# Kernel optimization log

Measured on AMD Instinct MI355X. Metric: run time of the kernel, lower is better.

## Reference

```python
import jax, jax.numpy as jnp
import numpy as np

EMBED_DIM = 768
NUM_HEADS = 12
HEAD_DIM = EMBED_DIM // NUM_HEADS
B, S = 2, 2048


def setup_inputs() -> dict:
    key = jax.random.key(0)
    ks = jax.random.split(key, 6)
    glorot = jnp.sqrt(6.0 / (EMBED_DIM + EMBED_DIM)).astype(jnp.float32)
    x = jax.random.normal(ks[0], (B, S, EMBED_DIM), dtype=jnp.float32)
    mask = jnp.zeros((1, 1, S, S), dtype=jnp.float32)  # additive mask, 0 = no masking
    Wq = jax.random.uniform(ks[1], (EMBED_DIM, EMBED_DIM), jnp.float32, -glorot, glorot)
    Wk = jax.random.uniform(ks[2], (EMBED_DIM, EMBED_DIM), jnp.float32, -glorot, glorot)
    Wv = jax.random.uniform(ks[3], (EMBED_DIM, EMBED_DIM), jnp.float32, -glorot, glorot)
    Wo = jax.random.uniform(ks[4], (EMBED_DIM, EMBED_DIM), jnp.float32, -glorot, glorot)
    bo = jnp.zeros((EMBED_DIM,), dtype=jnp.float32)
    return {"x": x, "mask": mask, "Wq": Wq, "Wk": Wk, "Wv": Wv, "Wo": Wo, "bo": bo}


def reference(x, mask, Wq, Wk, Wv, Wo, bo):
    b, s, _ = x.shape
    # Q/K/V projections (no bias), split into heads: [b, h, s, d]
    def split_heads(t):
        return t.reshape(b, s, NUM_HEADS, HEAD_DIM).transpose(0, 2, 1, 3)
    q = split_heads(x @ Wq)
    k = split_heads(x @ Wk)
    v = split_heads(x @ Wv)
    scale = 1.0 / jnp.sqrt(jnp.float32(HEAD_DIM))
    logits = jnp.einsum('bhqd,bhkd->bhqk', q, k) * scale  # [b, h, s, s]
    logits = logits + mask * (-1e9)
    weights = jax.nn.softmax(logits, axis=-1)
    attn = jnp.einsum('bhqk,bhkd->bhqd', weights, v)
    concat = attn.transpose(0, 2, 1, 3).reshape(b, s, EMBED_DIM)
    return concat @ Wo + bo
```

## Files before the change

### kernel.cpp

```cpp
#include <hip/hip_runtime.h>


typedef __bf16 bf16_t;
typedef bf16_t bf16x8 __attribute__((ext_vector_type(8)));
typedef bf16_t bf16x4 __attribute__((ext_vector_type(4)));
typedef float f32x4 __attribute__((ext_vector_type(4)));
typedef _Float16 f16x4 __attribute__((ext_vector_type(4)));
typedef _Float16 f16x8 __attribute__((ext_vector_type(8)));
typedef __fp16 hf2 __attribute__((ext_vector_type(2)));

#define SC2 0.1803368801111137f
#define DEFER_THR 44.0f

__device__ __forceinline__ float bf2f(unsigned short u) {
  union { unsigned int i; float f; } x;
  x.i = ((unsigned int)u) << 16;
  return x.f;
}

__device__ __forceinline__ float fexp2(float x) {
  return __builtin_amdgcn_exp2f(x);
}

__device__ __forceinline__ void glds16(const bf16_t* g, bf16_t* l) {
  __builtin_amdgcn_global_load_lds(
      (const __attribute__((address_space(1))) void*)g,
      (__attribute__((address_space(3))) void*)l, 16, 0, 0);
}

__device__ __forceinline__ int detect_bf16_flag(const unsigned short* x) {
  const int lane = threadIdx.x & 63;
  const uint4* p = (const uint4*)x;
  uint4 a = p[lane * 2];
  uint4 b = p[lane * 2 + 1];
  unsigned int w[8] = {a.x, a.y, a.z, a.w, b.x, b.y, b.z, b.w};
  unsigned int big = 0;
#pragma unroll
  for (int i = 0; i < 8; i++) {
    unsigned int e0 = (w[i] >> 7) & 0xFF, e1 = (w[i] >> 23) & 0xFF;
    big |= (e0 > 0x88u) | (e1 > 0x88u);
  }
  unsigned long long bal = __ballot(big != 0u);
  return bal == 0ULL ? 1 : 0;
}

__global__ void k_prep(const void* __restrict__ x, const void* __restrict__ mask,
                       const void* __restrict__ Wq, const void* __restrict__ Wk,
                       const void* __restrict__ Wv, const void* __restrict__ Wo,
                       bf16_t* __restrict__ xb, bf16_t* __restrict__ wqkvT,
                       bf16_t* __restrict__ woT, int* __restrict__ mflags) {
  __shared__ float ts[32][33];
  __shared__ int snz;
  const int blk = blockIdx.x;
  const int f = detect_bf16_flag((const unsigned short*)x);

  if (blk < 1536) {
    if (f) return;
    int i = blk * 256 + threadIdx.x;
    const float* xf = (const float*)x + (size_t)i * 8;
    bf16x8 v;
#pragma unroll
    for (int j = 0; j < 8; j++) v[j] = (bf16_t)xf[j];
    *(bf16x8*)(xb + (size_t)i * 8) = v;
  } else if (blk < 3840) {
    const int t = blk - 1536;
    const int z = t / 576, r = t % 576, kt = r / 24, nt = r % 24;
    const void* wsrc = (z == 0) ? Wq : (z == 1) ? Wk : (z == 2) ? Wv : Wo;
    bf16_t* dst = (z < 3) ? (wqkvT + (size_t)z * 768 * 768) : woT;
    const int c = threadIdx.x & 31, r0 = threadIdx.x >> 5;
#pragma unroll
    for (int i = 0; i < 4; i++) {
      int kr = kt * 32 + r0 + i * 8;
      float v;
      if (f) v = bf2f(((const unsigned short*)wsrc)[(size_t)kr * 768 + nt * 32 + c]);
      else   v = ((const float*)wsrc)[(size_t)kr * 768 + nt * 32 + c];
      ts[r0 + i * 8][c] = v;
    }
    __syncthreads();
#pragma unroll
    for (int i = 0; i < 4; i++) {
      int nr = nt * 32 + r0 + i * 8;
      dst[(size_t)nr * 768 + kt * 32 + c] = (bf16_t)ts[c][r0 + i * 8];
    }
  } else {
    const int t = blk - 3840;
    const int qt = t >> 4, ktm = t & 15;
    if (threadIdx.x == 0) snz = 0;
    __syncthreads();
    unsigned int nz = 0;
    if (f) {
#pragma unroll
      for (int i = 0; i < 8; i++) {
        int uidx = i * 256 + threadIdx.x;
        int row = uidx >> 4, col = uidx & 15;
        const uint4* p = (const uint4*)((const char*)mask +
            ((size_t)(qt * 128 + row) * 2048 + ktm * 128) * 2 + col * 16);
        uint4 v = *p;
        nz |= ((v.x | v.y | v.z | v.w) & 0x7fff7fffu);
      }
    } else {
#pragma unroll
      for (int i = 0; i < 16; i++) {
        int uidx = i * 256 + threadIdx.x;
        int row = uidx >> 5, col = uidx & 31;
        const uint4* p = (const uint4*)((const char*)mask +
            ((size_t)(qt * 128 + row) * 2048 + ktm * 128) * 4 + col * 16);
        uint4 v = *p;
        nz |= ((v.x | v.y | v.z | v.w) & 0x7fffffffu);
      }
    }
    if (nz) snz = 1;
    __syncthreads();
    if (threadIdx.x == 0) mflags[qt * 16 + ktm] = snz;
  }
}

__global__ __launch_bounds__(256, 3) void k_gemmQKV(
    const bf16_t* __restrict__ xb, const bf16_t* __restrict__ Bm,
    bf16_t* __restrict__ Qd, bf16_t* __restrict__ Kd, _Float16* __restrict__ Vt,
    const unsigned short* __restrict__ xdet) {
  __shared__ __align__(16) char smem[32768];
  _Float16* Tb = (_Float16*)smem;

  const int f = detect_bf16_flag(xdet);
  const bf16_t* A = f ? (const bf16_t*)xdet : xb;

  const int tid = threadIdx.x;
  const int n0 = blockIdx.x * 128, m0 = blockIdx.y * 128;
  const int r = tid >> 2, c8 = (tid & 3) << 3;
  const bf16_t* Ag = A + (size_t)(m0 + r) * 768 + c8;
  const bf16_t* Bg = Bm + (size_t)(n0 + r) * 768 + c8;
  const int wid = tid >> 6, lane = tid & 63;
  const int wm = (wid >> 1) << 6, wn = (wid & 1) << 6;
  const int lr = lane & 15, lk = (lane >> 4) << 3, g4 = (lane >> 4) << 2;

  f32x4 acc[4][4];
  const f32x4 z = {0.f, 0.f, 0.f, 0.f};
#pragma unroll
  for (int i = 0; i < 4; i++)
#pragma unroll
    for (int j = 0; j < 4; j++) acc[i][j] = z;

  {
    bf16_t* A0 = (bf16_t*)smem;
    bf16_t* B0 = (bf16_t*)(smem + 16384);
    glds16(Ag, A0 + wid * 512);
    glds16(Ag + (size_t)64 * 768, A0 + 2048 + wid * 512);
    glds16(Bg, B0 + wid * 512);
    glds16(Bg + (size_t)64 * 768, B0 + 2048 + wid * 512);
  }
  __syncthreads();

  for (int s = 0; s < 24; s++) {
    if (s < 23) {
      const int k0 = (s + 1) * 32;
      bf16_t* An = (bf16_t*)(smem + ((s + 1) & 1) * 8192);
      bf16_t* Bn = (bf16_t*)(smem + 16384 + ((s + 1) & 1) * 8192);
      glds16(Ag + k0, An + wid * 512);
      glds16(Ag + (size_t)64 * 768 + k0, An + 2048 + wid * 512);
      glds16(Bg + k0, Bn + wid * 512);
      glds16(Bg + (size_t)64 * 768 + k0, Bn + 2048 + wid * 512);
    }
    const bf16_t* As = (const bf16_t*)(smem + (s & 1) * 8192);
    const bf16_t* Bs = (const bf16_t*)(smem + 16384 + (s & 1) * 8192);
    bf16x8 af[4], bf_[4];
#pragma unroll
    for (int t = 0; t < 4; t++) af[t]  = *(const bf16x8*)&As[(wm + t * 16 + lr) * 32 + lk];
#pragma unroll
    for (int t = 0; t < 4; t++) bf_[t] = *(const bf16x8*)&Bs[(wn + t * 16 + lr) * 32 + lk];
#pragma unroll
    for (int i = 0; i < 4; i++)
#pragma unroll
      for (int j = 0; j < 4; j++)
        acc[i][j] = __builtin_amdgcn_mfma_f32_16x16x32_bf16(af[i], bf_[j], acc[i][j], 0, 0, 0);
    __syncthreads();
  }

  if (n0 < 1536) {
    bf16_t* dst = (n0 < 768) ? Qd : Kd;
    const int nb = (n0 < 768) ? n0 : n0 - 768;
    const int bb = m0 >> 11;
#pragma unroll
    for (int i = 0; i < 4; i++)
#pragma unroll
      for (int j = 0; j < 4; j++) {
        const int rc = nb + wn + j * 16 + lr;
        const int hh = rc >> 6, dd = rc & 63;
        const size_t base = (((size_t)bb * 12 + hh) * 2048) * 64 + dd;
#pragma unroll
        for (int reg = 0; reg < 4; reg++) {
          const int s = (m0 & 2047) + wm + i * 16 + g4 + reg;
          dst[base + (size_t)s * 64] = (bf16_t)acc[i][j][reg];
        }
      }
  } else {
    const int bb = m0 >> 11;
#pragma unroll
    for (int half = 0; half < 2; half++) {
      if ((wid & 1) == half) {
#pragma unroll
        for (int j = 0; j < 4; j++) {
          const int d_l = j * 16 + lr;
#pragma unroll
          for (int i = 0; i < 4; i++)
#pragma unroll
            for (int reg = 0; reg < 4; reg++)
              Tb[d_l * 136 + wm + i * 16 + g4 + reg] = (_Float16)acc[i][j][reg];
        }
      }
      __syncthreads();
      const int row = tid >> 2, cc = (tid & 3) * 32;
      const int vcol = (n0 - 1536) + half * 64 + row;
      const int hh = vcol >> 6;
      _Float16* dstv = Vt + (((size_t)bb * 12 + hh) * 64 + row) * 2048 + (m0 & 2047) + cc;
#pragma unroll
      for (int u = 0; u < 4; u++)
        *(uint4*)(dstv + u * 8) = *(const uint4*)&Tb[row * 136 + cc + u * 8];
      __syncthreads();
    }
  }
}

__global__ __launch_bounds__(320, 4) void k_flash(
    const bf16_t* __restrict__ Qd, const bf16_t* __restrict__ Kd,
    const _Float16* __restrict__ Vt, const void* __restrict__ mask,
    const int* __restrict__ mflags, const unsigned short* __restrict__ xdet,
    bf16_t* __restrict__ attn) {
  __shared__ __align__(16) char sm[32768];

  const int tid = threadIdx.x, wid = tid >> 6, lane = tid & 63;
  const int lr = lane & 15, quad = lane >> 4, lk = quad << 3, g4 = quad << 2;

  const int lin = blockIdx.x;
  const int gx = lin & 7, ww = lin >> 3;
  const int hb = gx * 3 + (ww >> 5);
  const int h = hb % 12, bb = hb / 12;
  const int qt = ww & 31;

  const size_t bh = (size_t)bb * 12 + h;
  const char* Kh = (const char*)(Kd + bh * 2048 * 64);
  const char* Vh = (const char*)(Vt + bh * 64 * 2048);

  if (wid == 4) {
    const char* kS[8]; const char* vS[8];
    int kL[8], vL[8];
#pragma unroll
    for (int u = 0; u < 8; u++) {
      const int R = (u >> 1) * 16 + lr;
      const int cG = (u & 1) * 4 + quad;
      kS[u] = Kh + R * 128 + cG * 16;
      const int s = ((u >> 2) << 5) + (((lr >> 2) & 1) << 4) +
                    (((u >> 1) & 1) << 3) + ((lr >> 3) << 2) + (lr & 3);
      kL[u] = (s >> 4) * 2048 + (cG & 3) * 256 + (s & 15) * 16 + (cG >> 2) * 1024;
      vS[u] = Vh + (size_t)lane * 4096 + u * 16;
      vL[u] = 8192 + lane * 128 + ((u * 16) ^ ((lane & 7) << 4));
    }
    uint4 kv[8], vv[8];
#pragma unroll
    for (int u = 0; u < 8; u++) kv[u] = *(const uint4*)(kS[u]);
#pragma unroll
    for (int u = 0; u < 8; u++) vv[u] = *(const uint4*)(vS[u]);
#pragma unroll
    for (int u = 0; u < 8; u++) *(uint4*)(sm + kL[u]) = kv[u];
#pragma unroll
    for (int u = 0; u < 8; u++) *(uint4*)(sm + vL[u]) = vv[u];
    __syncthreads();
    for (int s = 0; s < 32; s++) {
      if (s < 31) {
        const int t = s + 1;
        char* buf = sm + (t & 1) * 16384;
#pragma unroll
        for (int u = 0; u < 8; u++) kv[u] = *(const uint4*)(kS[u] + (size_t)t * 8192);
#pragma unroll
        for (int u = 0; u < 8; u++) vv[u] = *(const uint4*)(vS[u] + (size_t)t * 128);
#pragma unroll
        for (int u = 0; u < 8; u++) *(uint4*)(buf + kL[u]) = kv[u];
#pragma unroll
        for (int u = 0; u < 8; u++) *(uint4*)(buf + vL[u]) = vv[u];
      }
      __syncthreads();
    }
    return;
  }

  const bf16_t* Qh = Qd + bh * 2048 * 64;
  const int q0 = qt * 64 + wid * 16;
  const int mbf = detect_bf16_flag(xdet);
  const int* mfrow = mflags + (qt >> 1) * 16;
  int mbits = 0;
#pragma unroll
  for (int t = 0; t < 16; t++) mbits |= (mfrow[t] != 0) << t;

  const bf16x8 qf0 = *(const bf16x8*)&Qh[(size_t)(q0 + lr) * 64 + lk];
  const bf16x8 qf1 = *(const bf16x8*)&Qh[(size_t)(q0 + lr) * 64 + 32 + lk];

  f16x8 ones8;
#pragma unroll
  for (int j = 0; j < 8; j++) ones8[j] = (_Float16)1.f;

  const int vxo0 = (quad * 16) ^ ((lr & 7) << 4);
  const int vxo1 = (64 + quad * 16) ^ ((lr & 7) << 4);

  const f32x4 z = {0.f, 0.f, 0.f, 0.f};
  f32x4 ot[4];
#pragma unroll
  for (int dt = 0; dt < 4; dt++) ot[dt] = z;
  float mrow = -1e30f, lrow = 0.f;

  __syncthreads();

  for (int s = 0; s < 32; s++) {
    const char* Kc = sm + (s & 1) * 16384;
    const char* Vc = Kc + 8192;

    f32x4 sv[4];
#pragma unroll
    for (int ct = 0; ct < 4; ct++) sv[ct] = z;
    __builtin_amdgcn_s_setprio(1);
#pragma unroll
    for (int ct = 0; ct < 4; ct++) {
      bf16x8 kf0 = *(const bf16x8*)(Kc + ct * 2048 + lane * 16);
      bf16x8 kf1 = *(const bf16x8*)(Kc + ct * 2048 + 1024 + lane * 16);
      sv[ct] = __builtin_amdgcn_mfma_f32_16x16x32_bf16(kf0, qf0, sv[ct], 0, 0, 0);
      sv[ct] = __builtin_amdgcn_mfma_f32_16x16x32_bf16(kf1, qf1, sv[ct], 0, 0, 0);
    }
    __builtin_amdgcn_s_setprio(0);

    if ((mbits >> (s >> 1)) & 1) {
#pragma unroll
      for (int ct = 0; ct < 4; ct++)
#pragma unroll
        for (int reg = 0; reg < 4; reg++) {
          const int kk = ((ct >> 1) << 5) + (quad << 3) + ((ct & 1) << 2) + reg;
          size_t mi = (size_t)(q0 + lr) * 2048 + s * 64 + kk;
          float mv = mbf ? bf2f(((const unsigned short*)mask)[mi])
                         : ((const float*)mask)[mi];
          sv[ct][reg] -= 8e9f * mv;
        }
    }

    float t = fmaxf(
        fmaxf(fmaxf(fmaxf(sv[0][0], sv[0][1]), fmaxf(sv[0][2], sv[0][3])),
              fmaxf(fmaxf(sv[1][0], sv[1][1]), fmaxf(sv[1][2], sv[1][3]))),
        fmaxf(fmaxf(fmaxf(sv[2][0], sv[2][1]), fmaxf(sv[2][2], sv[2][3])),
              fmaxf(fmaxf(sv[3][0], sv[3][1]), fmaxf(sv[3][2], sv[3][3]))));
    t = fmaxf(t, __shfl_xor(t, 16));
    t = fmaxf(t, __shfl_xor(t, 32));
    if (__ballot(t > mrow + DEFER_THR)) {
      const float mnew = fmaxf(mrow, t);
      const float alpha = fexp2((mrow - mnew) * SC2);
#pragma unroll
      for (int dt = 0; dt < 4; dt++)
#pragma unroll
        for (int reg = 0; reg < 4; reg++) ot[dt][reg] *= alpha;
      lrow *= alpha;
      mrow = mnew;
    }
    const float mS = mrow * SC2;

    f16x8 pb8[2];
#pragma unroll
    for (int c2 = 0; c2 < 2; c2++) {
      union { hf2 h[4]; f16x8 v; } u;
#pragma unroll
      for (int hh2 = 0; hh2 < 2; hh2++) {
        const int ct = c2 * 2 + hh2;
        float p0 = fexp2(fmaf(sv[ct][0], SC2, -mS));
        float p1 = fexp2(fmaf(sv[ct][1], SC2, -mS));
        float p2 = fexp2(fmaf(sv[ct][2], SC2, -mS));
        float p3 = fexp2(fmaf(sv[ct][3], SC2, -mS));
        u.h[hh2 * 2 + 0] = __builtin_amdgcn_cvt_pkrtz(p0, p1);
        u.h[hh2 * 2 + 1] = __builtin_amdgcn_cvt_pkrtz(p2, p3);
      }
      pb8[c2] = u.v;
    }

    f32x4 asum = z;
    __builtin_amdgcn_s_setprio(1);
#pragma unroll
    for (int c2 = 0; c2 < 2; c2++) {
      const int vxo = c2 ? vxo1 : vxo0;
      asum = __builtin_amdgcn_mfma_f32_16x16x32_f16(ones8, pb8[c2], asum, 0, 0, 0);
#pragma unroll
      for (int dt = 0; dt < 4; dt++) {
        f16x8 va = *(const f16x8*)(Vc + (dt * 16 + lr) * 128 + vxo);
        ot[dt] = __builtin_amdgcn_mfma_f32_16x16x32_f16(va, pb8[c2], ot[dt], 0, 0, 0);
      }
    }
    __builtin_amdgcn_s_setprio(0);
    lrow += asum[0];
    __syncthreads();
  }

  const float inv = 1.0f / lrow;
  bf16_t* arow = attn + ((size_t)bb * 2048 + q0 + lr) * 768 + h * 64 + g4;
#pragma unroll
  for (int dt = 0; dt < 4; dt++) {
    bf16x4 v;
#pragma unroll
    for (int reg = 0; reg < 4; reg++) v[reg] = (bf16_t)(ot[dt][reg] * inv);
    *(bf16x4*)(arow + dt * 16) = v;
  }
}

__global__ __launch_bounds__(256, 3) void k_gemm2(
    const bf16_t* __restrict__ A, const bf16_t* __restrict__ Bm,
    const void* __restrict__ bo, const unsigned short* __restrict__ xdet,
    float* __restrict__ outF, unsigned short* __restrict__ outH) {
  __shared__ __align__(16) char smem[32768];

  const int tid = threadIdx.x, wid = tid >> 6, lane = tid & 63;
  const int n0 = blockIdx.x * 64, m0 = blockIdx.y * 64;
  const int wm = (wid >> 1) << 5, wn = (wid & 1) << 5;
  const int lr = lane & 15, lk = (lane >> 4) << 3, g4 = (lane >> 4) << 2;
  const bf16_t* Ag = A + (size_t)(m0 + (tid >> 2)) * 768 + ((tid & 3) << 3);
  const bf16_t* Bg = Bm + (size_t)(n0 + (tid >> 2)) * 768 + ((tid & 3) << 3);

  f32x4 acc[2][2];
  const f32x4 z = {0.f, 0.f, 0.f, 0.f};
#pragma unroll
  for (int i = 0; i < 2; i++)
#pragma unroll
    for (int j = 0; j < 2; j++) acc[i][j] = z;

  {
    bf16_t* A0 = (bf16_t*)smem;
    bf16_t* B0 = (bf16_t*)(smem + 16384);
    glds16(Ag, A0 + wid * 512);
    glds16(Ag + 32, A0 + 2048 + wid * 512);
    glds16(Bg, B0 + wid * 512);
    glds16(Bg + 32, B0 + 2048 + wid * 512);
  }
  __syncthreads();

  for (int s = 0; s < 12; s++) {
    if (s < 11) {
      const int k0 = (s + 1) * 64;
      bf16_t* An = (bf16_t*)(smem + ((s + 1) & 1) * 8192);
      bf16_t* Bn = (bf16_t*)(smem + 16384 + ((s + 1) & 1) * 8192);
      glds16(Ag + k0, An + wid * 512);
      glds16(Ag + k0 + 32, An + 2048 + wid * 512);
      glds16(Bg + k0, Bn + wid * 512);
      glds16(Bg + k0 + 32, Bn + 2048 + wid * 512);
    }
#pragma unroll
    for (int kc = 0; kc < 2; kc++) {
      const bf16_t* As = (const bf16_t*)(smem + (s & 1) * 8192) + kc * 2048;
      const bf16_t* Bs = (const bf16_t*)(smem + 16384 + (s & 1) * 8192) + kc * 2048;
      bf16x8 af[2], bf_[2];
#pragma unroll
      for (int i = 0; i < 2; i++) af[i]  = *(const bf16x8*)&As[(wm + i * 16 + lr) * 32 + lk];
#pragma unroll
      for (int j = 0; j < 2; j++) bf_[j] = *(const bf16x8*)&Bs[(wn + j * 16 + lr) * 32 + lk];
#pragma unroll
      for (int i = 0; i < 2; i++)
#pragma unroll
        for (int j = 0; j < 2; j++)
          acc[i][j] = __builtin_amdgcn_mfma_f32_16x16x32_bf16(af[i], bf_[j], acc[i][j], 0, 0, 0);
    }
    __syncthreads();
  }

  const int obf = detect_bf16_flag(xdet);
#pragma unroll
  for (int i = 0; i < 2; i++)
#pragma unroll
    for (int j = 0; j < 2; j++) {
      const int nn = n0 + wn + j * 16 + lr;
      const float bv = obf ? bf2f(((const unsigned short*)bo)[nn])
                           : ((const float*)bo)[nn];
#pragma unroll
      for (int reg = 0; reg < 4; reg++) {
        const int m = m0 + wm + i * 16 + g4 + reg;
        const float v = acc[i][j][reg] + bv;
        if (obf) outH[(size_t)m * 768 + nn] = __builtin_bit_cast(unsigned short, (bf16_t)v);
        else     outF[(size_t)m * 768 + nn] = v;
      }
    }
}

extern "C" void kernel_launch(void* const* d_in, const int* in_sizes, int n_in,
                              void* d_out, int out_size, void* d_ws, size_t ws_size,
                              hipStream_t stream) {
  (void)in_sizes; (void)n_in; (void)out_size; (void)ws_size;
  const void* x    = d_in[0];
  const void* mask = d_in[1];
  const void* Wq   = d_in[2];
  const void* Wk   = d_in[3];
  const void* Wv   = d_in[4];
  const void* Wo   = d_in[5];
  const void* bo   = d_in[6];

  char* w = (char*)d_ws;
  size_t off = 0;
  auto take = [&](size_t b) -> void* {
    void* p = w + off;
    off = (off + b + 255) & ~(size_t)255;
    return p;
  };
  int*      mflags = (int*)take(256 * 4);
  bf16_t*   wqkvT  = (bf16_t*)take((size_t)2304 * 768 * 2);
  bf16_t*   woT    = (bf16_t*)take((size_t)768 * 768 * 2);
  bf16_t*   xb     = (bf16_t*)take((size_t)4096 * 768 * 2);
  bf16_t*   Qd     = (bf16_t*)take((size_t)3145728 * 2);
  bf16_t*   Kd     = (bf16_t*)take((size_t)3145728 * 2);
  _Float16* Vt     = (_Float16*)take((size_t)3145728 * 2);
  bf16_t*   attn   = xb;

  k_prep<<<4096, 256, 0, stream>>>(x, mask, Wq, Wk, Wv, Wo, xb, wqkvT, woT, mflags);
  k_gemmQKV<<<dim3(18, 32), 256, 0, stream>>>(xb, wqkvT, Qd, Kd, Vt,
                                              (const unsigned short*)x);
  k_flash<<<768, 320, 0, stream>>>(Qd, Kd, Vt, mask, mflags,
                                   (const unsigned short*)x, attn);
  k_gemm2<<<dim3(12, 64), 256, 0, stream>>>(attn, woT, bo, (const unsigned short*)x,
                                            (float*)d_out, (unsigned short*)d_out);
}
```

Before: 178.1 us.

## Pre-swizzle K/V tiles in QKV GEMM epilogue and load via direct-to-LDS copies

The QKV GEMM epilogue now writes K and V into a tile-major layout that exactly matches the shared-memory layout the flash kernel consumes, including the swizzle. This lets the flash kernel drop its dedicated producer wave, which loaded into registers and stored to LDS, and instead have all four compute waves issue contiguous global-to-LDS 16-byte copies for the next tile. The intent is to cut the block from 320 to 256 threads, remove the register round trip and scattered address math, and let loads overlap compute through double buffering. In exchange, the GEMM epilogue now does scattered 2-byte stores for K, and the prefetch is issued by the compute waves themselves.

```diff
diff --git a/kernel.cpp b/kernel.cpp
--- a/kernel.cpp
+++ b/kernel.cpp
@@ -117,7 +117,7 @@
 
 __global__ __launch_bounds__(256, 3) void k_gemmQKV(
     const bf16_t* __restrict__ xb, const bf16_t* __restrict__ Bm,
-    bf16_t* __restrict__ Qd, bf16_t* __restrict__ Kd, _Float16* __restrict__ Vt,
+    bf16_t* __restrict__ Qd, char* __restrict__ Kd, char* __restrict__ Vt,
     const unsigned short* __restrict__ xdet) {
   __shared__ __align__(16) char smem[32768];
   _Float16* Tb = (_Float16*)smem;
@@ -132,7 +132,7 @@
   const bf16_t* Bg = Bm + (size_t)(n0 + r) * 768 + c8;
   const int wid = tid >> 6, lane = tid & 63;
   const int wm = (wid >> 1) << 6, wn = (wid & 1) << 6;
-  const int lr = lane & 15, lk = (lane >> 4) << 3, g4 = (lane >> 4) << 2;
+  const int lr = lane & 15, quad = lane >> 4, lk = quad << 3, g4 = quad << 2;
 
   f32x4 acc[4][4];
   const f32x4 z = {0.f, 0.f, 0.f, 0.f};
@@ -176,23 +176,42 @@
     __syncthreads();
   }
 
-  if (n0 < 1536) {
-    bf16_t* dst = (n0 < 768) ? Qd : Kd;
-    const int nb = (n0 < 768) ? n0 : n0 - 768;
+  if (n0 < 768) {
     const int bb = m0 >> 11;
 #pragma unroll
     for (int i = 0; i < 4; i++)
+#pragma unroll
+      for (int j = 0; j < 4; j++) {
+        const int rc = n0 + wn + j * 16 + lr;
+        const int hh = rc >> 6, dd = rc & 63;
+        const size_t base = (((size_t)bb * 12 + hh) * 2048) * 64 + dd;
+#pragma unroll
+        for (int reg = 0; reg < 4; reg++) {
+          const int s = (m0 & 2047) + wm + i * 16 + g4 + reg;
+          Qd[base + (size_t)s * 64] = (bf16_t)acc[i][j][reg];
+        }
+      }
+  } else if (n0 < 1536) {
+    const int nb = n0 - 768;
+    const int bb = m0 >> 11;
+    const int g = ((m0 & 2047) + wm) >> 6;
+#pragma unroll
+    for (int i = 0; i < 4; i++) {
 #pragma unroll
       for (int j = 0; j < 4; j++) {
         const int rc = nb + wn + j * 16 + lr;
         const int hh = rc >> 6, dd = rc & 63;
-        const size_t base = (((size_t)bb * 12 + hh) * 2048) * 64 + dd;
+        const size_t tbase = ((size_t)((bb * 12 + hh) * 32 + g)) << 13;
+        const int doff = ((dd >> 5) << 10) + (((dd >> 3) & 3) << 8) + ((dd & 7) << 1);
 #pragma unroll
         for (int reg = 0; reg < 4; reg++) {
-          const int s = (m0 & 2047) + wm + i * 16 + g4 + reg;
-          dst[base + (size_t)s * 64] = (bf16_t)acc[i][j][reg];
+          const int sig = ((i >> 1) << 5) + ((quad & 1) << 4) +
+                          (((((i & 1) << 1) | (quad >> 1))) << 2) + reg;
+          *(bf16_t*)(Kd + tbase + ((sig >> 4) << 11) + ((sig & 15) << 4) + doff) =
+              (bf16_t)acc[i][j][reg];
         }
       }
+    }
   } else {
     const int bb = m0 >> 11;
 #pragma unroll
@@ -212,18 +231,21 @@
       const int row = tid >> 2, cc = (tid & 3) * 32;
       const int vcol = (n0 - 1536) + half * 64 + row;
       const int hh = vcol >> 6;
-      _Float16* dstv = Vt + (((size_t)bb * 12 + hh) * 64 + row) * 2048 + (m0 & 2047) + cc;
+      const int g = ((m0 & 2047) + cc) >> 6;
+      const int koff2 = (cc & 63) * 2;
+      char* vb = Vt + (((size_t)((bb * 12 + hh) * 32 + g)) << 13) + (row << 7);
 #pragma unroll
       for (int u = 0; u < 4; u++)
-        *(uint4*)(dstv + u * 8) = *(const uint4*)&Tb[row * 136 + cc + u * 8];
+        *(uint4*)(vb + ((koff2 + u * 16) ^ ((row & 7) << 4))) =
+            *(const uint4*)&Tb[row * 136 + cc + u * 8];
       __syncthreads();
     }
   }
 }
 
-__global__ __launch_bounds__(320, 4) void k_flash(
-    const bf16_t* __restrict__ Qd, const bf16_t* __restrict__ Kd,
-    const _Float16* __restrict__ Vt, const void* __restrict__ mask,
+__global__ __launch_bounds__(256, 4) void k_flash(
+    const bf16_t* __restrict__ Qd, const char* __restrict__ Kd,
+    const char* __restrict__ Vt, const void* __restrict__ mask,
     const int* __restrict__ mflags, const unsigned short* __restrict__ xdet,
     bf16_t* __restrict__ attn) {
   __shared__ __align__(16) char sm[32768];
@@ -238,50 +260,22 @@
   const int qt = ww & 31;
 
   const size_t bh = (size_t)bb * 12 + h;
-  const char* Kh = (const char*)(Kd + bh * 2048 * 64);
-  const char* Vh = (const char*)(Vt + bh * 64 * 2048);
-
-  if (wid == 4) {
-    const char* kS[8]; const char* vS[8];
-    int kL[8], vL[8];
-#pragma unroll
-    for (int u = 0; u < 8; u++) {
-      const int R = (u >> 1) * 16 + lr;
-      const int cG = (u & 1) * 4 + quad;
-      kS[u] = Kh + R * 128 + cG * 16;
-      const int s = ((u >> 2) << 5) + (((lr >> 2) & 1) << 4) +
-                    (((u >> 1) & 1) << 3) + ((lr >> 3) << 2) + (lr & 3);
-      kL[u] = (s >> 4) * 2048 + (cG & 3) * 256 + (s & 15) * 16 + (cG >> 2) * 1024;
-      vS[u] = Vh + (size_t)lane * 4096 + u * 16;
-      vL[u] = 8192 + lane * 128 + ((u * 16) ^ ((lane & 7) << 4));
-    }
-    uint4 kv[8], vv[8];
-#pragma unroll
-    for (int u = 0; u < 8; u++) kv[u] = *(const uint4*)(kS[u]);
-#pragma unroll
-    for (int u = 0; u < 8; u++) vv[u] = *(const uint4*)(vS[u]);
-#pragma unroll
-    for (int u = 0; u < 8; u++) *(uint4*)(sm + kL[u]) = kv[u];
-#pragma unroll
-    for (int u = 0; u < 8; u++) *(uint4*)(sm + vL[u]) = vv[u];
-    __syncthreads();
-    for (int s = 0; s < 32; s++) {
-      if (s < 31) {
-        const int t = s + 1;
-        char* buf = sm + (t & 1) * 16384;
-#pragma unroll
-        for (int u = 0; u < 8; u++) kv[u] = *(const uint4*)(kS[u] + (size_t)t * 8192);
-#pragma unroll
-        for (int u = 0; u < 8; u++) vv[u] = *(const uint4*)(vS[u] + (size_t)t * 128);
-#pragma unroll
-        for (int u = 0; u < 8; u++) *(uint4*)(buf + kL[u]) = kv[u];
-#pragma unroll
-        for (int u = 0; u < 8; u++) *(uint4*)(buf + vL[u]) = vv[u];
-      }
-      __syncthreads();
-    }
-    return;
-  }
+  const char* Kg = Kd + (bh << 18);
+  const char* Vg = Vt + (bh << 18);
+
+  const char* kgl = Kg + wid * 2048 + lane * 16;
+  const char* vgl = Vg + wid * 2048 + lane * 16;
+
+#define STAGE(t, buf)                                                      \
+  {                                                                        \
+    const size_t o_ = (size_t)(t) * 8192;                                  \
+    glds16((const bf16_t*)(kgl + o_),        (bf16_t*)((buf) + wid * 2048));        \
+    glds16((const bf16_t*)(kgl + o_ + 1024), (bf16_t*)((buf) + wid * 2048 + 1024)); \
+    glds16((const bf16_t*)(vgl + o_),        (bf16_t*)((buf) + 8192 + wid * 2048)); \
+    glds16((const bf16_t*)(vgl + o_ + 1024), (bf16_t*)((buf) + 8192 + wid * 2048 + 1024)); \
+  }
+
+  STAGE(0, sm);
 
   const bf16_t* Qh = Qd + bh * 2048 * 64;
   const int q0 = qt * 64 + wid * 16;
@@ -310,7 +304,9 @@
   __syncthreads();
 
   for (int s = 0; s < 32; s++) {
-    const char* Kc = sm + (s & 1) * 16384;
+    if (s < 31) STAGE(s + 1, sm + (((s + 1) & 1) << 14));
+
+    const char* Kc = sm + ((s & 1) << 14);
     const char* Vc = Kc + 8192;
 
     f32x4 sv[4];
@@ -391,6 +387,7 @@
     lrow += asum[0];
     __syncthreads();
   }
+#undef STAGE
 
   const float inv = 1.0f / lrow;
   bf16_t* arow = attn + ((size_t)bb * 2048 + q0 + lr) * 768 + h * 64 + g4;
@@ -503,14 +500,14 @@
   bf16_t*   woT    = (bf16_t*)take((size_t)768 * 768 * 2);
   bf16_t*   xb     = (bf16_t*)take((size_t)4096 * 768 * 2);
   bf16_t*   Qd     = (bf16_t*)take((size_t)3145728 * 2);
-  bf16_t*   Kd     = (bf16_t*)take((size_t)3145728 * 2);
-  _Float16* Vt     = (_Float16*)take((size_t)3145728 * 2);
+  char*     Kd     = (char*)take((size_t)3145728 * 2);
+  char*     Vt     = (char*)take((size_t)3145728 * 2);
   bf16_t*   attn   = xb;
 
   k_prep<<<4096, 256, 0, stream>>>(x, mask, Wq, Wk, Wv, Wo, xb, wqkvT, woT, mflags);
   k_gemmQKV<<<dim3(18, 32), 256, 0, stream>>>(xb, wqkvT, Qd, Kd, Vt,
                                               (const unsigned short*)x);
-  k_flash<<<768, 320, 0, stream>>>(Qd, Kd, Vt, mask, mflags,
+  k_flash<<<768, 256, 0, stream>>>(Qd, Kd, Vt, mask, mflags,
                                    (const unsigned short*)x, attn);
   k_gemm2<<<dim3(12, 64), 256, 0, stream>>>(attn, woT, bo, (const unsigned short*)x,
                                             (float*)d_out, (unsigned short*)d_out);
```

After: 172.2 us. -3.3%, faster.
